# Performance work log

Measured on AMD Instinct MI355X. Metric: run time of the kernel, lower is better.

Reference implementation:

```python
import jax, jax.numpy as jnp
import numpy as np
from jax import lax

B, NOBJ, NKEEP, D, HID, KS = 256, 100, 36, 2048, 1024, 256
H2 = HID // 2


def setup_inputs() -> dict:
    key = jax.random.key(0)
    ks = jax.random.split(key, 12)
    xy = jax.random.uniform(ks[0], (B, 2, NOBJ))
    wh = jax.random.uniform(ks[1], (B, 2, NOBJ)) * 0.5
    boxes = jnp.concatenate([xy, xy + wh], axis=1)  # [B,4,NOBJ], valid x1y1x2y2
    attention_orig = jax.random.normal(ks[2], (B, NOBJ))
    visual_feature = jax.random.normal(ks[3], (B, D, 1, NOBJ))
    v_origin = jax.random.normal(ks[4], (B, D, 1, NOBJ))
    que_type = jax.random.randint(ks[5], (B,), 0, 65)
    sD = 1.0 / np.sqrt(D)
    sH = 1.0 / np.sqrt(H2)
    Wv_score = jax.random.normal(ks[6], (D, KS)) * sD
    Wb_score = jax.random.normal(ks[7], (4, KS)) * 0.5
    Wx_up = jax.random.normal(ks[8], (D, 4 * H2)) * sD
    Wh_up = jax.random.normal(ks[9], (H2, 4 * H2)) * sH
    b_up = jnp.zeros((4 * H2,))
    Wx_dn = jax.random.normal(ks[10], (D, 4 * H2)) * sD
    Wh_dn = jax.random.normal(ks[11], (H2, 4 * H2)) * sH
    b_dn = jnp.zeros((4 * H2,))
    return dict(boxes=boxes, attention_orig=attention_orig, visual_feature=visual_feature,
                v_origin=v_origin, que_type=que_type, Wv_score=Wv_score, Wb_score=Wb_score,
                Wx_up=Wx_up, Wh_up=Wh_up, b_up=b_up, Wx_dn=Wx_dn, Wh_dn=Wh_dn, b_dn=b_dn)


def _cell(pre, c_prev):
    i, f, g, o = jnp.split(pre, 4, axis=-1)
    c = jax.nn.sigmoid(i) * jnp.tanh(g) + jax.nn.sigmoid(f) * c_prev
    return jax.nn.sigmoid(o) * jnp.tanh(c), c


def _forward(boxes, attention_orig, visual_feature, v_origin, que_type,
             Wv_score, Wb_score, Wx_up, Wh_up, b_up, Wx_dn, Wh_dn, b_dn):
    bidx = jnp.arange(B)
    # --- filter_most_important: keep top-NKEEP proposals by attention ---
    att_top, idx = lax.top_k(attention_orig, NKEEP)  # [B,NKEEP]
    vf = visual_feature.reshape(B, D, NOBJ)
    vo = v_origin.reshape(B, D, NOBJ)
    gD = jnp.broadcast_to(idx[:, None, :], (B, D, NKEEP))
    vf = jnp.take_along_axis(vf, gD, axis=2)
    vo = jnp.take_along_axis(vo, gD, axis=2)
    bx = jnp.take_along_axis(boxes, jnp.broadcast_to(idx[:, None, :], (B, 4, NKEEP)), axis=2)
    # --- arbitrary_trees_transfer: relevancy = outer product of sigmoid(att) ---
    att = jax.nn.sigmoid(att_top)
    relevancy = att[:, :, None] * att[:, None, :]  # [B,N,N]
    # gen_tree_net: pairwise scores from features + boxes
    f = jnp.tanh(jnp.einsum('bdn,dk->bnk', vo, Wv_score) + jnp.einsum('bdn,dk->bnk', bx, Wb_score))
    scores = jax.nn.sigmoid(jnp.einsum('bik,bjk->bij', f, f) / np.sqrt(KS))
    S = scores * relevancy  # edge weights for tree generation
    # --- deterministic maximum-spanning-tree (Prim) forest generation ---
    root = jnp.argmax(att_top, axis=1).astype(jnp.int32)
    in_tree0 = jnp.arange(NKEEP)[None, :] == root[:, None]  # [B,N] bool
    parent0 = jnp.full((B, NKEEP), NKEEP, dtype=jnp.int32)  # sentinel = NKEEP

    def prim_step(carry, _):
        in_tree, parent = carry
        cand = jnp.where(in_tree[:, :, None] & (~in_tree[:, None, :]), S, -jnp.inf)
        k = jnp.argmax(cand.reshape(B, -1), axis=1)
        p = (k // NKEEP).astype(jnp.int32)
        c = (k % NKEEP).astype(jnp.int32)
        in_tree = in_tree.at[bidx, c].set(True)
        parent = parent.at[bidx, c].set(p)
        return (in_tree, parent), c

    (_, parent), chs = lax.scan(prim_step, (in_tree0, parent0), None, length=NKEEP - 1)
    order = jnp.concatenate([root[None, :], chs], axis=0).T  # [B,NKEEP], topo order

    # --- bidirectional TreeLSTM over the forest ---
    x = jnp.swapaxes(vf, 1, 2)  # [B,N,D]
    xWu = x @ Wx_up + b_up      # [B,N,4*H2]
    xWd = x @ Wx_dn + b_dn

    # bottom-up (child-sum): reverse topo order, parents see summed child states
    h_up0 = jnp.zeros((B, NKEEP, H2))
    hsum0 = jnp.zeros((B, NKEEP + 1, H2))
    csum0 = jnp.zeros((B, NKEEP + 1, H2))

    def up_step(carry, t):
        h_up, hsum, csum = carry
        node = order[bidx, t]
        pre = xWu[bidx, node] + hsum[bidx, node] @ Wh_up
        h, c = _cell(pre, csum[bidx, node])
        h_up = h_up.at[bidx, node].set(h)
        par = parent[bidx, node]
        hsum = hsum.at[bidx, par].add(h)
        csum = csum.at[bidx, par].add(c)
        return (h_up, hsum, csum), None

    (h_up, _, _), _ = lax.scan(up_step, (h_up0, hsum0, csum0), jnp.arange(NKEEP - 1, -1, -1))

    # top-down: topo order, child sees parent's state (root sees zeros via sentinel)
    hd0 = jnp.zeros((B, NKEEP + 1, H2))
    cd0 = jnp.zeros((B, NKEEP + 1, H2))

    def dn_step(carry, t):
        hd, cd = carry
        node = order[bidx, t]
        par = parent[bidx, node]
        pre = xWd[bidx, node] + hd[bidx, par] @ Wh_dn
        h, c = _cell(pre, cd[bidx, par])
        hd = hd.at[bidx, node].set(h)
        cd = cd.at[bidx, node].set(c)
        return (hd, cd), None

    (hd, _), _ = lax.scan(dn_step, (hd0, cd0), jnp.arange(NKEEP))

    vh = jnp.concatenate([h_up, hd[:, :NKEEP]], axis=-1)  # [B,N,HID]
    return jnp.swapaxes(vh, 1, 2).reshape(B, HID, 1, NKEEP)


def reference(boxes, attention_orig, visual_feature, v_origin, que_type,
              Wv_score, Wb_score, Wx_up, Wh_up, b_up, Wx_dn, Wh_dn, b_dn):
    return _forward(boxes, attention_orig, visual_feature, v_origin, que_type,
                    Wv_score, Wb_score, Wx_up, Wh_up, b_up, Wx_dn, Wh_dn, b_dn)
```

## Files before the change

### kernel.cpp

```cpp
#include <hip/hip_runtime.h>
#include <math.h>

#define BB 256
#define NOBJ 100
#define NKEEP 36
#define DD 2048
#define HID 1024
#define KS 256
#define H2 512
#define NP1 (NKEEP + 1)
#define N4H 2048
#define FDS 8

typedef __attribute__((ext_vector_type(8))) short short8v;
typedef __attribute__((ext_vector_type(4))) float f32x4;
typedef unsigned short ushort_t;
typedef unsigned int uint_t;

__device__ __forceinline__ float sigf(float x) { return 1.0f / (1.0f + expf(-x)); }
__device__ __forceinline__ ushort_t f2b(float f) {
  uint_t u = __float_as_uint(f);
  uint_t r = (u + 0x7FFFu + ((u >> 16) & 1u)) >> 16;
  return (ushort_t)r;
}
__device__ __forceinline__ float b2f(ushort_t u) {
  return __uint_as_float(((uint_t)u) << 16);
}
__device__ __forceinline__ short8v pack8(float4 a, float4 b) {
  short8v p;
  p[0] = (short)f2b(a.x); p[1] = (short)f2b(a.y);
  p[2] = (short)f2b(a.z); p[3] = (short)f2b(a.w);
  p[4] = (short)f2b(b.x); p[5] = (short)f2b(b.y);
  p[6] = (short)f2b(b.z); p[7] = (short)f2b(b.w);
  return p;
}

#define GLOAD_LDS16(gp, lp)                                                   \
  __builtin_amdgcn_global_load_lds(                                           \
      (const __attribute__((address_space(1))) void*)(gp),                    \
      (__attribute__((address_space(3))) void*)(lp), 16, 0, 0)

__global__ __launch_bounds__(128) void topk_kernel(
    const float* __restrict__ att, const float* __restrict__ boxes,
    int* __restrict__ idx, float* __restrict__ att_sig,
    float* __restrict__ bxk, int* __restrict__ parent) {
  int b = blockIdx.x;
  int t = threadIdx.x;
  __shared__ float a[NOBJ];
  if (t < NOBJ) a[t] = att[b * NOBJ + t];
  __syncthreads();
  if (t < NOBJ) {
    float ai = a[t];
    int rank = 0;
    for (int j = 0; j < NOBJ; j++) {
      float aj = a[j];
      rank += (aj > ai) || (aj == ai && j < t);
    }
    if (rank < NKEEP) {
      idx[b * NKEEP + rank] = t;
      att_sig[b * NKEEP + rank] = 1.0f / (1.0f + expf(-ai));
      for (int c = 0; c < 4; c++)
        bxk[(b * NKEEP + rank) * 4 + c] = boxes[(b * 4 + c) * NOBJ + t];
    }
  }
  if (t < NKEEP) parent[b * NKEEP + t] = NKEEP;
}

__global__ __launch_bounds__(256) void gather_x(
    const float* __restrict__ vf, const int* __restrict__ idx,
    ushort_t* __restrict__ A2) {
  int b = blockIdx.x;
  int ksh = blockIdx.y;
  int d0 = ksh * 32;
  __shared__ float s[32][101];
  __shared__ int idxs[NKEEP];
  int tid = threadIdx.x;
  if (tid < NKEEP) idxs[tid] = idx[b * NKEEP + tid];
  for (int l = tid; l < 32 * NOBJ; l += 256) {
    int dd = l / NOBJ, c = l % NOBJ;
    s[dd][c] = vf[((size_t)b * DD + d0 + dd) * NOBJ + c];
  }
  __syncthreads();
  if (tid < NKEEP * 4) {
    int n = tid >> 2, q = tid & 3;
    int m = b * NKEEP + n;
    int mt = m >> 7, r = m & 127, g = r >> 4, row16 = r & 15;
    int cix = idxs[n];
    float v[8];
#pragma unroll
    for (int j = 0; j < 8; ++j) v[j] = s[q * 8 + j][cix];
    float4 va = make_float4(v[0], v[1], v[2], v[3]);
    float4 vb = make_float4(v[4], v[5], v[6], v[7]);
    size_t base = ((size_t)mt * 64 + ksh) * 4096 + g * 512 + (row16 + q * 16) * 8;
    *(short8v*)&A2[base] = pack8(va, vb);
  }
}

__global__ __launch_bounds__(256) void f_partial(
    const float* __restrict__ vo, const float* __restrict__ Wv,
    const int* __restrict__ idx, float* __restrict__ fpart) {
  int b = blockIdx.x;
  int ds = blockIdx.y;
  int k = threadIdx.x;
  __shared__ int idxs[NKEEP];
  __shared__ float vs[16][NKEEP];
  if (k < NKEEP) idxs[k] = idx[b * NKEEP + k];
  __syncthreads();
  float acc[NKEEP];
#pragma unroll
  for (int n = 0; n < NKEEP; n++) acc[n] = 0.0f;
  int dbeg = ds * (DD / FDS);
  for (int d0 = dbeg; d0 < dbeg + DD / FDS; d0 += 16) {
    __syncthreads();
    for (int l = k; l < 16 * NKEEP; l += 256) {
      int dd = l / NKEEP, n = l % NKEEP;
      vs[dd][n] = vo[((size_t)b * DD + d0 + dd) * NOBJ + idxs[n]];
    }
    __syncthreads();
#pragma unroll
    for (int dd = 0; dd < 16; dd++) {
      float w = Wv[(size_t)(d0 + dd) * KS + k];
#pragma unroll
      for (int n = 0; n < NKEEP; n++) acc[n] += vs[dd][n] * w;
    }
  }
  float* op = &fpart[(((size_t)ds * BB + b) * NKEEP) * KS + k];
#pragma unroll
  for (int n = 0; n < NKEEP; n++) op[n * KS] = acc[n];
}

__global__ __launch_bounds__(256) void f_combine(
    const float* __restrict__ fpart, const float* __restrict__ Wb,
    const float* __restrict__ bxk, float* __restrict__ fmat) {
  int b = blockIdx.x;
  int k = threadIdx.x;
  for (int n = 0; n < NKEEP; n++) {
    float s = 0.0f;
#pragma unroll
    for (int ds = 0; ds < FDS; ds++)
      s += fpart[(((size_t)ds * BB + b) * NKEEP + n) * KS + k];
#pragma unroll
    for (int c = 0; c < 4; c++) s += bxk[(b * NKEEP + n) * 4 + c] * Wb[c * KS + k];
    fmat[((size_t)b * NKEEP + n) * KS + k] = tanhf(s);
  }
}

__global__ __launch_bounds__(256) void s_kernel(
    const float* __restrict__ fmat, const float* __restrict__ att_sig,
    float* __restrict__ S) {
  int b = blockIdx.x;
  int tid = threadIdx.x;
  __shared__ float fs[NKEEP][KS + 1];
  __shared__ float as[NKEEP];
  for (int l = tid; l < NKEEP * KS; l += 256) {
    int n = l / KS, k = l % KS;
    fs[n][k] = fmat[((size_t)b * NKEEP + n) * KS + k];
  }
  if (tid < NKEEP) as[tid] = att_sig[b * NKEEP + tid];
  __syncthreads();
  for (int p = tid; p < NKEEP * NKEEP; p += 256) {
    int i = p / NKEEP, j = p % NKEEP;
    double acc = 0.0;
    for (int k = 0; k < KS; k++) acc += (double)fs[i][k] * (double)fs[j][k];
    float sc = 1.0f / (1.0f + expf(-(float)(acc * (1.0 / 16.0))));
    S[((size_t)b * NKEEP + i) * NKEEP + j] = sc * as[i] * as[j];
  }
}

__global__ __launch_bounds__(64) void prim_kernel(
    const float* __restrict__ S, int* __restrict__ parent,
    int* __restrict__ order) {
  int b = blockIdx.x;
  int lane = threadIdx.x;
  __shared__ float Ss[NKEEP * NKEEP];
  for (int l = lane; l < NKEEP * NKEEP; l += 64) Ss[l] = S[(size_t)b * NKEEP * NKEEP + l];
  __syncthreads();
  unsigned long long mask = 1ull;
  if (lane == 0) order[b * NKEEP + 0] = 0;
  for (int step = 1; step < NKEEP; step++) {
    float bv = -1.0f;
    int bk = NKEEP * NKEEP;
    for (int l = lane; l < NKEEP * NKEEP; l += 64) {
      int p = l / NKEEP, c = l % NKEEP;
      if (((mask >> p) & 1ull) && !((mask >> c) & 1ull)) {
        float v = Ss[l];
        if (v > bv || (v == bv && l < bk)) { bv = v; bk = l; }
      }
    }
    for (int off = 32; off > 0; off >>= 1) {
      float ov = __shfl_down(bv, off);
      int ok = __shfl_down(bk, off);
      if (ov > bv || (ov == bv && ok < bk)) { bv = ov; bk = ok; }
    }
    bk = __shfl(bk, 0);
    int p = bk / NKEEP, c = bk % NKEEP;
    mask |= (1ull << c);
    if (lane == 0) {
      parent[b * NKEEP + c] = p;
      order[b * NKEEP + step] = c;
    }
  }
}

__global__ __launch_bounds__(256) void wconv(
    const float* __restrict__ Wu, const float* __restrict__ Wd,
    ushort_t* __restrict__ B2) {
  int nt = blockIdx.x;
  int ks = blockIdx.y;
  int tid = threadIdx.x;
  const float* W = (nt < 16) ? Wu : Wd;
  int n0 = (nt & 15) * 128;
  int k0 = ks * 32;
  __shared__ float tile[32][129];
  for (int l = tid; l < 32 * 128; l += 256) {
    int kk = l >> 7, c = l & 127;
    tile[kk][c] = W[(size_t)(k0 + kk) * N4H + n0 + c];
  }
  __syncthreads();
  size_t obase = ((size_t)nt * 64 + ks) * 4096 + tid * 16;
  ushort_t ob[16];
#pragma unroll
  for (int u = 0; u < 16; u++) {
    int e = tid * 16 + u;
    int h = e >> 9;
    int lane = (e >> 3) & 63;
    int j = e & 7;
    int c = h * 16 + (lane & 15);
    int kk = (lane >> 4) * 8 + j;
    ob[u] = f2b(tile[kk][c]);
  }
  short8v o0, o1;
#pragma unroll
  for (int u = 0; u < 8; ++u) { o0[u] = (short)ob[u]; o1[u] = (short)ob[u + 8]; }
  *(short8v*)&B2[obase] = o0;
  *(short8v*)&B2[obase + 8] = o1;
}

__global__ __launch_bounds__(256) void whpack(
    const float* __restrict__ Wh, ushort_t* __restrict__ Wpk) {
  int s = blockIdx.x;
  int fg = blockIdx.y;
  __shared__ float tile[32][257];
  int tid = threadIdx.x;
  for (int l = tid; l < 32 * 64; l += 256) {
    int row = l >> 6, c4 = (l & 63) * 4;
    float4 v = *(const float4*)&Wh[(size_t)(32 * s + row) * N4H + fg * 256 + c4];
    tile[row][c4] = v.x; tile[row][c4 + 1] = v.y;
    tile[row][c4 + 2] = v.z; tile[row][c4 + 3] = v.w;
  }
  __syncthreads();
#pragma unroll
  for (int it = 0; it < 4; it++) {
    int cid = it * 256 + tid;
    int ff = cid >> 6, lane = cid & 63;
    int f = fg * 16 + ff;
    int col = ff * 16 + (lane & 15);
    int rbase = (lane >> 4) * 8;
    short8v p;
#pragma unroll
    for (int j = 0; j < 8; j++) p[j] = (short)f2b(tile[rbase + j][col]);
    *(short8v*)&Wpk[(((size_t)s * 128 + f) * 64 + lane) * 8] = p;
  }
}

__global__ __launch_bounds__(256) void mfma_gemm(
    const ushort_t* __restrict__ A2, const ushort_t* __restrict__ B2,
    const float* __restrict__ bu, const float* __restrict__ bd,
    float* __restrict__ Cu, float* __restrict__ Cd) {
  __shared__ __align__(16) ushort_t Asl[2][4096];
  __shared__ __align__(16) ushort_t Bsl[2][4096];
  int bid = blockIdx.x;
  int nt = bid & 31;
  int mt = bid >> 5;
  int tid = threadIdx.x;
  int w = tid >> 6, lane = tid & 63;
  int wr = w >> 1, wc = w & 1;
  f32x4 acc[4][4];
#pragma unroll
  for (int i = 0; i < 4; i++)
#pragma unroll
    for (int j = 0; j < 4; j++) acc[i][j] = (f32x4){0.f, 0.f, 0.f, 0.f};

  const ushort_t* ag =
      A2 + (size_t)mt * 64 * 4096 + (w * 2) * 512 + (size_t)lane * 8;
  const ushort_t* bg =
      B2 + (size_t)nt * 64 * 4096 + (w * 2) * 512 + (size_t)lane * 8;
  ushort_t* as0 = &Asl[0][(w * 2) * 512];
  ushort_t* bs0 = &Bsl[0][(w * 2) * 512];
  ushort_t* as1 = &Asl[1][(w * 2) * 512];
  ushort_t* bs1 = &Bsl[1][(w * 2) * 512];

  GLOAD_LDS16(ag, as0);
  GLOAD_LDS16(ag + 512, as0 + 512);
  GLOAD_LDS16(bg, bs0);
  GLOAD_LDS16(bg + 512, bs0 + 512);
  __syncthreads();
  for (int s = 0; s < 64; ++s) {
    int cur = s & 1;
    if (s < 63) {
      ag += 4096;
      bg += 4096;
      ushort_t* asd = cur ? as0 : as1;
      ushort_t* bsd = cur ? bs0 : bs1;
      GLOAD_LDS16(ag, asd);
      GLOAD_LDS16(ag + 512, asd + 512);
      GLOAD_LDS16(bg, bsd);
      GLOAD_LDS16(bg + 512, bsd + 512);
    }
    short8v a[4], bfr[4];
#pragma unroll
    for (int mi = 0; mi < 4; mi++)
      a[mi] = *(const short8v*)&Asl[cur][(wr * 4 + mi) * 512 + lane * 8];
#pragma unroll
    for (int ni = 0; ni < 4; ni++)
      bfr[ni] = *(const short8v*)&Bsl[cur][(wc * 4 + ni) * 512 + lane * 8];
#pragma unroll
    for (int mi = 0; mi < 4; mi++)
#pragma unroll
      for (int ni = 0; ni < 4; ni++)
        acc[mi][ni] = __builtin_amdgcn_mfma_f32_16x16x32_bf16(
            a[mi], bfr[ni], acc[mi][ni], 0, 0, 0);
    __syncthreads();
  }
  int col16 = lane & 15, rq = lane >> 4;
#pragma unroll
  for (int ni = 0; ni < 4; ni++) {
    int nglob = nt * 128 + wc * 64 + ni * 16 + col16;
    const float* bias = (nt < 16) ? bu : bd;
    float* C = (nt < 16) ? Cu : Cd;
    int nn = (nt < 16) ? nglob : nglob - N4H;
    float bv = bias[nn];
#pragma unroll
    for (int mi = 0; mi < 4; mi++) {
#pragma unroll
      for (int r = 0; r < 4; r++) {
        int m = mt * 128 + wr * 64 + mi * 16 + rq * 4 + r;
        C[(size_t)m * N4H + nn] = acc[mi][ni][r] + bv;
      }
    }
  }
}

__global__ __launch_bounds__(256, 2) void lstm_step(
    int i,
    const float* __restrict__ xWu, const float* __restrict__ xWd,
    const ushort_t* __restrict__ Wpku, const ushort_t* __restrict__ Wpkd,
    const int* __restrict__ order, const int* __restrict__ parent,
    float* __restrict__ hsum, float* __restrict__ csum,
    float* __restrict__ hup, float* __restrict__ hd, float* __restrict__ cd) {
  int bid = blockIdx.x;
  int bt = bid >> 5;
  int pkt = bid & 31;
  bool isdn = pkt >= 16;
  int kt = pkt & 15;
  int t = isdn ? i : (NKEEP - 1 - i);
  const float* xW = isdn ? xWd : xWu;
  const ushort_t* Wpk = isdn ? Wpkd : Wpku;

  __shared__ __align__(16) ushort_t Apk[16 * 64 * 8];
  __shared__ float pre[16][4][32];
  __shared__ int nodes[16], pars[16];

  int tid = threadIdx.x;
  if (tid < 16) {
    int b = bt * 16 + tid;
    int nd = order[b * NKEEP + t];
    nodes[tid] = nd;
    pars[tid] = parent[b * NKEEP + nd];
  }
  __syncthreads();
  {
    int bl = tid >> 4, r = tid & 15;
    int b = bt * 16 + bl;
    int rowi = isdn ? pars[bl] : nodes[bl];
    const float* asrc = isdn ? &hd[((size_t)b * NP1 + rowi) * H2 + r * 32]
                             : &hsum[((size_t)b * NP1 + rowi) * H2 + r * 32];
    float4 v0 = *(const float4*)&asrc[0];
    float4 v1 = *(const float4*)&asrc[4];
    float4 v2 = *(const float4*)&asrc[8];
    float4 v3 = *(const float4*)&asrc[12];
    float4 v4 = *(const float4*)&asrc[16];
    float4 v5 = *(const float4*)&asrc[20];
    float4 v6 = *(const float4*)&asrc[24];
    float4 v7 = *(const float4*)&asrc[28];
    int x = r & 7;
    *(short8v*)&Apk[((r * 64 + bl + 0) ^ x) * 8] = pack8(v0, v1);
    *(short8v*)&Apk[((r * 64 + bl + 16) ^ x) * 8] = pack8(v2, v3);
    *(short8v*)&Apk[((r * 64 + bl + 32) ^ x) * 8] = pack8(v4, v5);
    *(short8v*)&Apk[((r * 64 + bl + 48) ^ x) * 8] = pack8(v6, v7);
  }
  __syncthreads();
  int w = tid >> 6, lane = tid & 63;
  int col16 = lane & 15, rq = lane >> 4;
  {
    f32x4 acc0 = (f32x4){0.f, 0.f, 0.f, 0.f};
    f32x4 acc1 = (f32x4){0.f, 0.f, 0.f, 0.f};
    int f0 = w * 32 + kt * 2;
#pragma unroll
    for (int s = 0; s < 16; ++s) {
      short8v a = *(const short8v*)&Apk[((s * 64 + lane) ^ (s & 7)) * 8];
      short8v b0 = *(const short8v*)&Wpk[(((size_t)s * 128 + f0) * 64 + lane) * 8];
      short8v b1 = *(const short8v*)&Wpk[(((size_t)s * 128 + f0 + 1) * 64 + lane) * 8];
      acc0 = __builtin_amdgcn_mfma_f32_16x16x32_bf16(a, b0, acc0, 0, 0, 0);
      acc1 = __builtin_amdgcn_mfma_f32_16x16x32_bf16(a, b1, acc1, 0, 0, 0);
    }
#pragma unroll
    for (int r = 0; r < 4; ++r) {
      pre[rq * 4 + r][w][col16] = acc0[r];
      pre[rq * 4 + r][w][16 + col16] = acc1[r];
    }
  }
  __syncthreads();
  {
    int bl = tid >> 4, kc = (tid & 15) * 2;
    int b = bt * 16 + bl;
    int nd = nodes[bl], pr = pars[bl];
    int k = kt * 32 + kc;
    const float* xwb = &xW[((size_t)b * NKEEP + nd) * N4H + k];
    const float* cpsrc = isdn ? &cd[((size_t)b * NP1 + pr) * H2 + k]
                              : &csum[((size_t)b * NP1 + nd) * H2 + k];
    float2 cp = *(const float2*)cpsrc;
    float hv[2], cv[2];
#pragma unroll
    for (int e = 0; e < 2; ++e) {
      float pi = pre[bl][0][kc + e] + xwb[e];
      float pf = pre[bl][1][kc + e] + xwb[H2 + e];
      float pg = pre[bl][2][kc + e] + xwb[2 * H2 + e];
      float po = pre[bl][3][kc + e] + xwb[3 * H2 + e];
      float cprev = e ? cp.y : cp.x;
      float c = sigf(pi) * tanhf(pg) + sigf(pf) * cprev;
      hv[e] = sigf(po) * tanhf(c);
      cv[e] = c;
    }
    if (!isdn) {
      *(float2*)&hup[((size_t)b * NKEEP + nd) * H2 + k] = make_float2(hv[0], hv[1]);
      float* hsp = &hsum[((size_t)b * NP1 + pr) * H2 + k];
      float* csp = &csum[((size_t)b * NP1 + pr) * H2 + k];
      hsp[0] += hv[0]; hsp[1] += hv[1];
      csp[0] += cv[0]; csp[1] += cv[1];
    } else {
      *(float2*)&hd[((size_t)b * NP1 + nd) * H2 + k] = make_float2(hv[0], hv[1]);
      *(float2*)&cd[((size_t)b * NP1 + nd) * H2 + k] = make_float2(cv[0], cv[1]);
    }
  }
}

__global__ __launch_bounds__(256) void out_transpose(
    const float* __restrict__ hup, const float* __restrict__ hd,
    float* __restrict__ out) {
  int b = blockIdx.x;
  __shared__ float s[NKEEP][65];
  for (int half = 0; half < 2; half++) {
    const float* src = half ? hd : hup;
    int rs = half ? NP1 : NKEEP;
    for (int q0 = 0; q0 < H2; q0 += 64) {
      __syncthreads();
      for (int l = threadIdx.x; l < NKEEP * 64; l += 256) {
        int n = l / 64, qq = l % 64;
        s[n][qq] = src[((size_t)b * rs + n) * H2 + q0 + qq];
      }
      __syncthreads();
      for (int l = threadIdx.x; l < NKEEP * 64; l += 256) {
        int qq = l / NKEEP, n = l % NKEEP;
        out[(size_t)b * (HID * NKEEP) + (half * H2 + q0 + qq) * NKEEP + n] = s[n][qq];
      }
    }
  }
}

extern "C" void kernel_launch(void* const* d_in, const int* in_sizes, int n_in,
                              void* d_out, int out_size, void* d_ws, size_t ws_size,
                              hipStream_t stream) {
  const float* boxes = (const float*)d_in[0];
  const float* attention = (const float*)d_in[1];
  const float* vf = (const float*)d_in[2];
  const float* vo = (const float*)d_in[3];
  const float* Wv = (const float*)d_in[5];
  const float* Wb = (const float*)d_in[6];
  const float* Wx_up = (const float*)d_in[7];
  const float* Wh_up = (const float*)d_in[8];
  const float* b_up = (const float*)d_in[9];
  const float* Wx_dn = (const float*)d_in[10];
  const float* Wh_dn = (const float*)d_in[11];
  const float* b_dn = (const float*)d_in[12];
  float* out = (float*)d_out;

  char* ws = (char*)d_ws;
  size_t off = 0;
  auto take = [&](size_t bytes) -> char* {
    char* p = ws + off;
    off = (off + bytes + 255) & ~(size_t)255;
    return p;
  };
  int* idx = (int*)take((size_t)BB * NKEEP * 4);
  float* att_sig = (float*)take((size_t)BB * NKEEP * 4);
  float* bxk = (float*)take((size_t)BB * NKEEP * 4 * 4);
  int* parent = (int*)take((size_t)BB * NKEEP * 4);
  int* order = (int*)take((size_t)BB * NKEEP * 4);
  float* fmat = (float*)take((size_t)BB * NKEEP * KS * 4);
  float* S = (float*)take((size_t)BB * NKEEP * NKEEP * 4);
  ushort_t* A2 = (ushort_t*)take((size_t)72 * 64 * 4096 * 2);
  ushort_t* B2 = (ushort_t*)take((size_t)32 * 64 * 4096 * 2);
  float* xWu = (float*)take((size_t)BB * NKEEP * N4H * 4);
  float* xWd = (float*)take((size_t)BB * NKEEP * N4H * 4);
  float* hsum = (float*)take((size_t)BB * NP1 * H2 * 4);
  float* csum = (float*)take((size_t)BB * NP1 * H2 * 4);
  float* hd = (float*)take((size_t)BB * NP1 * H2 * 4);
  float* cd = (float*)take((size_t)BB * NP1 * H2 * 4);
  ushort_t* Wpku = (ushort_t*)take((size_t)16 * 128 * 64 * 8 * 2);
  ushort_t* Wpkd = (ushort_t*)take((size_t)16 * 128 * 64 * 8 * 2);
  float* hup = (float*)A2;
  float* fpart = xWd;

  topk_kernel<<<BB, 128, 0, stream>>>(attention, boxes, idx, att_sig, bxk, parent);
  gather_x<<<dim3(BB, 64), 256, 0, stream>>>(vf, idx, A2);
  f_partial<<<dim3(BB, FDS), 256, 0, stream>>>(vo, Wv, idx, fpart);
  f_combine<<<BB, 256, 0, stream>>>(fpart, Wb, bxk, fmat);
  s_kernel<<<BB, 256, 0, stream>>>(fmat, att_sig, S);
  prim_kernel<<<BB, 64, 0, stream>>>(S, parent, order);

  wconv<<<dim3(32, 64), 256, 0, stream>>>(Wx_up, Wx_dn, B2);
  whpack<<<dim3(16, 8), 256, 0, stream>>>(Wh_up, Wpku);
  whpack<<<dim3(16, 8), 256, 0, stream>>>(Wh_dn, Wpkd);

  mfma_gemm<<<72 * 32, 256, 0, stream>>>(A2, B2, b_up, b_dn, xWu, xWd);

  size_t accb = (size_t)BB * NP1 * H2 * 4;
  hipMemsetAsync(hsum, 0, accb * 4, stream);

  for (int i = 0; i < NKEEP; ++i)
    lstm_step<<<512, 256, 0, stream>>>(i, xWu, xWd, Wpku, Wpkd, order, parent,
                                       hsum, csum, hup, hd, cd);

  out_transpose<<<BB, 256, 0, stream>>>(hup, hd, out);
}
```

Baseline: 1.008 ms.

## Split LSTM step across twice as many blocks and fuse f_combine into s_kernel

Each lstm_step block now computes 16 hidden columns instead of 32, doubling the grid to 1024 blocks and raising the occupancy hint to 4 blocks per CU. This is meant to spread the latency-bound recurrent step over more CUs, at the cost of each block re-staging the same A tile, so redundant h loads and packing double. Separately, f_combine and s_kernel are merged so the tanh features stay in shared memory, removing one launch and the fmat global round trip.

Measured after the change: 1.086 ms. +7.8%, slower.

```diff
diff --git a/kernel.cpp b/kernel.cpp
--- a/kernel.cpp
+++ b/kernel.cpp
@@ -129,11 +129,14 @@
   for (int n = 0; n < NKEEP; n++) op[n * KS] = acc[n];
 }
 
-__global__ __launch_bounds__(256) void f_combine(
+__global__ __launch_bounds__(256) void fs_kernel(
     const float* __restrict__ fpart, const float* __restrict__ Wb,
-    const float* __restrict__ bxk, float* __restrict__ fmat) {
+    const float* __restrict__ bxk, const float* __restrict__ att_sig,
+    float* __restrict__ S) {
   int b = blockIdx.x;
   int k = threadIdx.x;
+  __shared__ float fs[NKEEP][KS + 1];
+  __shared__ float as[NKEEP];
   for (int n = 0; n < NKEEP; n++) {
     float s = 0.0f;
 #pragma unroll
@@ -141,27 +144,14 @@
       s += fpart[(((size_t)ds * BB + b) * NKEEP + n) * KS + k];
 #pragma unroll
     for (int c = 0; c < 4; c++) s += bxk[(b * NKEEP + n) * 4 + c] * Wb[c * KS + k];
-    fmat[((size_t)b * NKEEP + n) * KS + k] = tanhf(s);
-  }
-}
-
-__global__ __launch_bounds__(256) void s_kernel(
-    const float* __restrict__ fmat, const float* __restrict__ att_sig,
-    float* __restrict__ S) {
-  int b = blockIdx.x;
-  int tid = threadIdx.x;
-  __shared__ float fs[NKEEP][KS + 1];
-  __shared__ float as[NKEEP];
-  for (int l = tid; l < NKEEP * KS; l += 256) {
-    int n = l / KS, k = l % KS;
-    fs[n][k] = fmat[((size_t)b * NKEEP + n) * KS + k];
-  }
-  if (tid < NKEEP) as[tid] = att_sig[b * NKEEP + tid];
-  __syncthreads();
-  for (int p = tid; p < NKEEP * NKEEP; p += 256) {
+    fs[n][k] = tanhf(s);
+  }
+  if (k < NKEEP) as[k] = att_sig[b * NKEEP + k];
+  __syncthreads();
+  for (int p = k; p < NKEEP * NKEEP; p += 256) {
     int i = p / NKEEP, j = p % NKEEP;
     double acc = 0.0;
-    for (int k = 0; k < KS; k++) acc += (double)fs[i][k] * (double)fs[j][k];
+    for (int kk = 0; kk < KS; kk++) acc += (double)fs[i][kk] * (double)fs[j][kk];
     float sc = 1.0f / (1.0f + expf(-(float)(acc * (1.0 / 16.0))));
     S[((size_t)b * NKEEP + i) * NKEEP + j] = sc * as[i] * as[j];
   }
@@ -341,7 +331,7 @@
   }
 }
 
-__global__ __launch_bounds__(256, 2) void lstm_step(
+__global__ __launch_bounds__(256, 4) void lstm_step(
     int i,
     const float* __restrict__ xWu, const float* __restrict__ xWd,
     const ushort_t* __restrict__ Wpku, const ushort_t* __restrict__ Wpkd,
@@ -349,16 +339,16 @@
     float* __restrict__ hsum, float* __restrict__ csum,
     float* __restrict__ hup, float* __restrict__ hd, float* __restrict__ cd) {
   int bid = blockIdx.x;
-  int bt = bid >> 5;
-  int pkt = bid & 31;
-  bool isdn = pkt >= 16;
-  int kt = pkt & 15;
+  int bt = bid >> 6;
+  int pkt = bid & 63;
+  bool isdn = pkt >= 32;
+  int kt = pkt & 31;
   int t = isdn ? i : (NKEEP - 1 - i);
   const float* xW = isdn ? xWd : xWu;
   const ushort_t* Wpk = isdn ? Wpkd : Wpku;
 
   __shared__ __align__(16) ushort_t Apk[16 * 64 * 8];
-  __shared__ float pre[16][4][32];
+  __shared__ float pre[16][4][16];
   __shared__ int nodes[16], pars[16];
 
   int tid = threadIdx.x;
@@ -394,53 +384,38 @@
   int col16 = lane & 15, rq = lane >> 4;
   {
     f32x4 acc0 = (f32x4){0.f, 0.f, 0.f, 0.f};
-    f32x4 acc1 = (f32x4){0.f, 0.f, 0.f, 0.f};
-    int f0 = w * 32 + kt * 2;
+    int f0 = w * 32 + kt;
 #pragma unroll
     for (int s = 0; s < 16; ++s) {
       short8v a = *(const short8v*)&Apk[((s * 64 + lane) ^ (s & 7)) * 8];
       short8v b0 = *(const short8v*)&Wpk[(((size_t)s * 128 + f0) * 64 + lane) * 8];
-      short8v b1 = *(const short8v*)&Wpk[(((size_t)s * 128 + f0 + 1) * 64 + lane) * 8];
       acc0 = __builtin_amdgcn_mfma_f32_16x16x32_bf16(a, b0, acc0, 0, 0, 0);
-      acc1 = __builtin_amdgcn_mfma_f32_16x16x32_bf16(a, b1, acc1, 0, 0, 0);
-    }
-#pragma unroll
-    for (int r = 0; r < 4; ++r) {
-      pre[rq * 4 + r][w][col16] = acc0[r];
-      pre[rq * 4 + r][w][16 + col16] = acc1[r];
-    }
+    }
+#pragma unroll
+    for (int r = 0; r < 4; ++r) pre[rq * 4 + r][w][col16] = acc0[r];
   }
   __syncthreads();
   {
-    int bl = tid >> 4, kc = (tid & 15) * 2;
+    int bl = tid >> 4, kc = tid & 15;
     int b = bt * 16 + bl;
     int nd = nodes[bl], pr = pars[bl];
-    int k = kt * 32 + kc;
+    int k = kt * 16 + kc;
     const float* xwb = &xW[((size_t)b * NKEEP + nd) * N4H + k];
-    const float* cpsrc = isdn ? &cd[((size_t)b * NP1 + pr) * H2 + k]
-                              : &csum[((size_t)b * NP1 + nd) * H2 + k];
-    float2 cp = *(const float2*)cpsrc;
-    float hv[2], cv[2];
-#pragma unroll
-    for (int e = 0; e < 2; ++e) {
-      float pi = pre[bl][0][kc + e] + xwb[e];
-      float pf = pre[bl][1][kc + e] + xwb[H2 + e];
-      float pg = pre[bl][2][kc + e] + xwb[2 * H2 + e];
-      float po = pre[bl][3][kc + e] + xwb[3 * H2 + e];
-      float cprev = e ? cp.y : cp.x;
-      float c = sigf(pi) * tanhf(pg) + sigf(pf) * cprev;
-      hv[e] = sigf(po) * tanhf(c);
-      cv[e] = c;
-    }
+    float cprev = isdn ? cd[((size_t)b * NP1 + pr) * H2 + k]
+                       : csum[((size_t)b * NP1 + nd) * H2 + k];
+    float pi = pre[bl][0][kc] + xwb[0];
+    float pf = pre[bl][1][kc] + xwb[H2];
+    float pg = pre[bl][2][kc] + xwb[2 * H2];
+    float po = pre[bl][3][kc] + xwb[3 * H2];
+    float c = sigf(pi) * tanhf(pg) + sigf(pf) * cprev;
+    float hv = sigf(po) * tanhf(c);
     if (!isdn) {
-      *(float2*)&hup[((size_t)b * NKEEP + nd) * H2 + k] = make_float2(hv[0], hv[1]);
-      float* hsp = &hsum[((size_t)b * NP1 + pr) * H2 + k];
-      float* csp = &csum[((size_t)b * NP1 + pr) * H2 + k];
-      hsp[0] += hv[0]; hsp[1] += hv[1];
-      csp[0] += cv[0]; csp[1] += cv[1];
+      hup[((size_t)b * NKEEP + nd) * H2 + k] = hv;
+      hsum[((size_t)b * NP1 + pr) * H2 + k] += hv;
+      csum[((size_t)b * NP1 + pr) * H2 + k] += c;
     } else {
-      *(float2*)&hd[((size_t)b * NP1 + nd) * H2 + k] = make_float2(hv[0], hv[1]);
-      *(float2*)&cd[((size_t)b * NP1 + nd) * H2 + k] = make_float2(cv[0], cv[1]);
+      hd[((size_t)b * NP1 + nd) * H2 + k] = hv;
+      cd[((size_t)b * NP1 + nd) * H2 + k] = c;
     }
   }
 }
@@ -497,7 +472,6 @@
   float* bxk = (float*)take((size_t)BB * NKEEP * 4 * 4);
   int* parent = (int*)take((size_t)BB * NKEEP * 4);
   int* order = (int*)take((size_t)BB * NKEEP * 4);
-  float* fmat = (float*)take((size_t)BB * NKEEP * KS * 4);
   float* S = (float*)take((size_t)BB * NKEEP * NKEEP * 4);
   ushort_t* A2 = (ushort_t*)take((size_t)72 * 64 * 4096 * 2);
   ushort_t* B2 = (ushort_t*)take((size_t)32 * 64 * 4096 * 2);
@@ -515,8 +489,7 @@
   topk_kernel<<<BB, 128, 0, stream>>>(attention, boxes, idx, att_sig, bxk, parent);
   gather_x<<<dim3(BB, 64), 256, 0, stream>>>(vf, idx, A2);
   f_partial<<<dim3(BB, FDS), 256, 0, stream>>>(vo, Wv, idx, fpart);
-  f_combine<<<BB, 256, 0, stream>>>(fpart, Wb, bxk, fmat);
-  s_kernel<<<BB, 256, 0, stream>>>(fmat, att_sig, S);
+  fs_kernel<<<BB, 256, 0, stream>>>(fpart, Wb, bxk, att_sig, S);
   prim_kernel<<<BB, 64, 0, stream>>>(S, parent, order);
 
   wconv<<<dim3(32, 64), 256, 0, stream>>>(Wx_up, Wx_dn, B2);
@@ -529,8 +502,8 @@
   hipMemsetAsync(hsum, 0, accb * 4, stream);
 
   for (int i = 0; i < NKEEP; ++i)
-    lstm_step<<<512, 256, 0, stream>>>(i, xWu, xWd, Wpku, Wpkd, order, parent,
-                                       hsum, csum, hup, hd, cd);
+    lstm_step<<<1024, 256, 0, stream>>>(i, xWu, xWd, Wpku, Wpkd, order, parent,
+                                        hsum, csum, hup, hd, cd);
 
   out_transpose<<<BB, 256, 0, stream>>>(hup, hd, out);
 }
```
